# Kernel tuning notes

Hardware: AMD Instinct MI355X
Metric: run time of the kernel (lower is better)

The kernel has to match this reference:

```python
import jax, jax.numpy as jnp
import numpy as np

B, N, F_IN, F_OUT = 8, 2048, 256, 256
NEG_SLOPE = 0.2
EPS = 1e-7


def setup_inputs() -> dict:
    key = jax.random.key(0)
    k1, k2, k3, k4, k5 = jax.random.split(key, 5)
    x = jax.random.normal(k1, (B, N, F_IN), dtype=jnp.float32)
    # A is a 0/1 adjacency mask used as float in the module
    A = jax.random.bernoulli(k2, 0.5, (B, N, N)).astype(jnp.float32)
    # W: xavier_normal_ init, shape [in_features, out_features]
    W = jax.random.normal(k3, (F_IN, F_OUT), dtype=jnp.float32) * np.sqrt(2.0 / (F_IN + F_OUT))
    # attention_mechanism: Linear(2*F_OUT, 1) -> weight vector [2*F_OUT], scalar bias
    bound = 1.0 / np.sqrt(2 * F_OUT)
    a_w = jax.random.uniform(k4, (2 * F_OUT,), dtype=jnp.float32, minval=-bound, maxval=bound)
    a_b = jax.random.uniform(k5, (), dtype=jnp.float32, minval=-bound, maxval=bound)
    return {"A": A, "x": x, "W": W, "a_w": a_w, "a_b": a_b}


def reference(A, x, W, a_w, a_b):
    # Wh = x @ W : [B, N, F_OUT]
    Wh = jnp.einsum('bnf,fo->bno', x, W)
    # Linear([Wh_i ; Wh_j]) == Wh_i @ a_w[:F] + Wh_j @ a_w[F:] + b  (no O(N^2 F) concat)
    s_src = Wh @ a_w[:F_OUT]   # [B, N] contribution of row index i
    s_dst = Wh @ a_w[F_OUT:]   # [B, N] contribution of col index j
    e = s_src[:, :, None] + s_dst[:, None, :] + a_b  # [B, N, N]
    e = jnp.where(e > 0, e, NEG_SLOPE * e)           # leaky_relu(0.2)
    # masked softmax over dim=1 (as in the original module)
    exps = jnp.exp(e) * A
    sums = jnp.sum(exps, axis=1, keepdims=True) + EPS
    attn = exps / sums                                # [B, N, N]
    return jnp.einsum('bij,bjo->bio', attn, Wh)       # [B, N, F_OUT]
```

## Files before the change

kernel.cpp:

```cpp
#include <hip/hip_runtime.h>
#include <hip/hip_bf16.h>

#define NN 2048
#define BB 8
#define FD 256
#define NEG_SLOPE 0.2f
#define EPSV 1e-7f
#define PSTR 40

typedef __bf16 bf16x8 __attribute__((ext_vector_type(8)));
typedef __bf16 bf16x4 __attribute__((ext_vector_type(4)));
typedef float f32x4 __attribute__((ext_vector_type(4)));

__global__ __launch_bounds__(256) void k1_prep(const float* __restrict__ W,
                                               __bf16* __restrict__ WT) {
    int idx = blockIdx.x * 256 + threadIdx.x;
    int o = idx >> 8, f = idx & 255;
    WT[idx] = (__bf16)W[f * FD + o];
}

__global__ __launch_bounds__(256) void k2_whgemm(const float* __restrict__ x,
                                                 const __bf16* __restrict__ WT,
                                                 float* __restrict__ Wh) {
    const int wave = threadIdx.x >> 6;
    const int lane = threadIdx.x & 63;
    const int row0 = blockIdx.x * 32 + (wave >> 1) * 16;
    const int ohalf = (wave & 1) * 128;
    const int m = lane & 15;
    const int quad = lane >> 4;
    const int row = row0 + m;
    const float* xrow = x + (size_t)row * FD + quad * 8;

    f32x4 acc[8];
#pragma unroll
    for (int n = 0; n < 8; ++n) acc[n] = (f32x4){0.f, 0.f, 0.f, 0.f};

    for (int k0 = 0; k0 < FD; k0 += 32) {
        float4 xa = *(const float4*)(xrow + k0);
        float4 xb = *(const float4*)(xrow + k0 + 4);
        bf16x8 af;
        af[0] = (__bf16)xa.x; af[1] = (__bf16)xa.y; af[2] = (__bf16)xa.z; af[3] = (__bf16)xa.w;
        af[4] = (__bf16)xb.x; af[5] = (__bf16)xb.y; af[6] = (__bf16)xb.z; af[7] = (__bf16)xb.w;
#pragma unroll
        for (int n = 0; n < 8; ++n) {
            int o = ohalf + n * 16 + m;
            bf16x8 bf = *(const bf16x8*)(WT + o * FD + k0 + quad * 8);
            acc[n] = __builtin_amdgcn_mfma_f32_16x16x32_bf16(af, bf, acc[n], 0, 0, 0);
        }
    }
#pragma unroll
    for (int n = 0; n < 8; ++n) {
        int o = ohalf + n * 16 + m;
#pragma unroll
        for (int r = 0; r < 4; ++r) {
            Wh[(size_t)(row0 + quad * 4 + r) * FD + o] = acc[n][r];
        }
    }
}

__global__ __launch_bounds__(256) void k3_scores(const float* __restrict__ Wh,
                                                 const float* __restrict__ a_w,
                                                 float* __restrict__ s_src,
                                                 float* __restrict__ s_dst) {
    int wave = threadIdx.x >> 6, lane = threadIdx.x & 63;
    int row = blockIdx.x * 4 + wave;
    float4 wv = *(const float4*)(Wh + (size_t)row * FD + lane * 4);
    float4 a0 = *(const float4*)(a_w + lane * 4);
    float4 a1 = *(const float4*)(a_w + FD + lane * 4);
    float d0 = wv.x * a0.x + wv.y * a0.y + wv.z * a0.z + wv.w * a0.w;
    float d1 = wv.x * a1.x + wv.y * a1.y + wv.z * a1.z + wv.w * a1.w;
#pragma unroll
    for (int off = 32; off; off >>= 1) {
        d0 += __shfl_down(d0, off, 64);
        d1 += __shfl_down(d1, off, 64);
    }
    if (lane == 0) { s_src[row] = d0; s_dst[row] = d1; }
}

__global__ __launch_bounds__(256) void k4_den(const float* __restrict__ A,
                                              const float* __restrict__ s_src,
                                              const float* __restrict__ s_dst,
                                              const float* __restrict__ a_bp,
                                              float* __restrict__ den_part) {
    const int blk = blockIdx.x;
    const int b = blk & 7;
    const int jhalf = (blk >> 3) & 1;
    const int isp = blk >> 4;
    const int i0 = isp * 32;
    const int j = jhalf * 1024 + threadIdx.x * 4;
    __shared__ float ss[32];
    if (threadIdx.x < 32) ss[threadIdx.x] = s_src[b * NN + i0 + threadIdx.x] + a_bp[0];
    __syncthreads();
    float4 sd = *(const float4*)(s_dst + b * NN + j);
    float ax = 0.f, ay = 0.f, az = 0.f, aw = 0.f;
    const float* Ap = A + ((size_t)b * NN + i0) * NN + j;
#pragma unroll 8
    for (int i = 0; i < 32; ++i) {
        float4 a = *(const float4*)(Ap + (size_t)i * NN);
        float si = ss[i];
        float e0 = si + sd.x; e0 = e0 > 0.f ? e0 : NEG_SLOPE * e0;
        float e1 = si + sd.y; e1 = e1 > 0.f ? e1 : NEG_SLOPE * e1;
        float e2 = si + sd.z; e2 = e2 > 0.f ? e2 : NEG_SLOPE * e2;
        float e3 = si + sd.w; e3 = e3 > 0.f ? e3 : NEG_SLOPE * e3;
        ax += a.x * __expf(e0);
        ay += a.y * __expf(e1);
        az += a.z * __expf(e2);
        aw += a.w * __expf(e3);
    }
    float4 r = (float4){ax, ay, az, aw};
    *(float4*)(den_part + (size_t)isp * (BB * NN) + b * NN + j) = r;
}

__global__ __launch_bounds__(256) void k5_wht(const float* __restrict__ Wh,
                                              const float* __restrict__ den_part,
                                              __bf16* __restrict__ WhT) {
    const int b = blockIdx.z;
    const int j0 = blockIdx.x * 64;
    const int o0 = blockIdx.y * 64;
    __shared__ float tile[64][65];
    __shared__ float invd[64];
    if (threadIdx.x < 64) {
        float s = 0.f;
        const float* dp = den_part + b * NN + j0 + threadIdx.x;
#pragma unroll 8
        for (int sI = 0; sI < 64; ++sI) s += dp[(size_t)sI * (BB * NN)];
        invd[threadIdx.x] = 1.f / (s + EPSV);
    }
    __syncthreads();
    int jr = threadIdx.x >> 4, oc = (threadIdx.x & 15) * 4;
#pragma unroll
    for (int p = 0; p < 4; ++p) {
        int jj = jr + p * 16;
        float4 v = *(const float4*)(Wh + (size_t)(b * NN + j0 + jj) * FD + o0 + oc);
        float s = invd[jj];
        tile[jj][oc + 0] = v.x * s;
        tile[jj][oc + 1] = v.y * s;
        tile[jj][oc + 2] = v.z * s;
        tile[jj][oc + 3] = v.w * s;
    }
    __syncthreads();
    int ow = threadIdx.x >> 4, jc = (threadIdx.x & 15) * 4;
#pragma unroll
    for (int p = 0; p < 4; ++p) {
        int o = ow + p * 16;
        bf16x4 wv;
        wv[0] = (__bf16)tile[jc + 0][o];
        wv[1] = (__bf16)tile[jc + 1][o];
        wv[2] = (__bf16)tile[jc + 2][o];
        wv[3] = (__bf16)tile[jc + 3][o];
        *(bf16x4*)(WhT + (size_t)(b * FD + o0 + o) * NN + j0 + jc) = wv;
    }
}

__global__ __launch_bounds__(512, 4) void k6_out(const float* __restrict__ A,
                                                 const __bf16* __restrict__ WhT,
                                                 const float* __restrict__ s_src,
                                                 const float* __restrict__ s_dst,
                                                 const float* __restrict__ a_bp,
                                                 float* __restrict__ part) {
    __shared__ __bf16 P[2][128 * PSTR];
    const int blk = blockIdx.x;
    const int b = blk & 7;
    const int r_ = blk >> 3;
    const int itile = r_ & 15;
    const int jsp = r_ >> 4;
    const int i0 = itile * 128;
    const int jbase = jsp * 512;
    const int t = threadIdx.x;
    const int w = t >> 6, lane = t & 63;
    const int wrow = w >> 2, wcol = w & 3;
    const int m = lane & 15, quad = lane >> 4;

    const int prow = t >> 2, ps = t & 3;
    const float ssr = s_src[b * NN + i0 + prow] + a_bp[0];
    const float* Abase = A + ((size_t)(b * NN + i0 + prow)) * NN + jbase + ps * 8;
    const float* sdbase = s_dst + b * NN + jbase + ps * 8;
    __bf16* Pw = &P[0][0] + prow * PSTR + ps * 8;

    float4 a0 = *(const float4*)(Abase);
    float4 a1 = *(const float4*)(Abase + 4);
    float4 q0 = *(const float4*)(sdbase);
    float4 q1 = *(const float4*)(sdbase + 4);

#define BUILD_P(dstbuf)                                                          \
    {                                                                            \
        bf16x8 wv; float e;                                                      \
        e = ssr + q0.x; e = e > 0.f ? e : NEG_SLOPE * e; wv[0] = (__bf16)(a0.x * __expf(e)); \
        e = ssr + q0.y; e = e > 0.f ? e : NEG_SLOPE * e; wv[1] = (__bf16)(a0.y * __expf(e)); \
        e = ssr + q0.z; e = e > 0.f ? e : NEG_SLOPE * e; wv[2] = (__bf16)(a0.z * __expf(e)); \
        e = ssr + q0.w; e = e > 0.f ? e : NEG_SLOPE * e; wv[3] = (__bf16)(a0.w * __expf(e)); \
        e = ssr + q1.x; e = e > 0.f ? e : NEG_SLOPE * e; wv[4] = (__bf16)(a1.x * __expf(e)); \
        e = ssr + q1.y; e = e > 0.f ? e : NEG_SLOPE * e; wv[5] = (__bf16)(a1.y * __expf(e)); \
        e = ssr + q1.z; e = e > 0.f ? e : NEG_SLOPE * e; wv[6] = (__bf16)(a1.z * __expf(e)); \
        e = ssr + q1.w; e = e > 0.f ? e : NEG_SLOPE * e; wv[7] = (__bf16)(a1.w * __expf(e)); \
        *(bf16x8*)(Pw + (dstbuf) * (128 * PSTR)) = wv;                           \
    }

    BUILD_P(0)

    f32x4 acc[4][4];
#pragma unroll
    for (int r = 0; r < 4; ++r)
#pragma unroll
        for (int n = 0; n < 4; ++n) acc[r][n] = (f32x4){0.f, 0.f, 0.f, 0.f};

    const __bf16* Bbase = WhT + (size_t)(b * FD + wcol * 64 + m) * NN + jbase + quad * 8;
    const __bf16* Prd = &P[0][0] + (wrow * 64 + m) * PSTR + quad * 8;

    for (int kk = 0; kk < 16; ++kk) {
        __syncthreads();
        if (kk < 15) {
            const float* An = Abase + (kk + 1) * 32;
            const float* Sn = sdbase + (kk + 1) * 32;
            a0 = *(const float4*)(An);
            a1 = *(const float4*)(An + 4);
            q0 = *(const float4*)(Sn);
            q1 = *(const float4*)(Sn + 4);
        }
        const __bf16* Pk = Prd + (kk & 1) * (128 * PSTR);
        bf16x8 af[4];
#pragma unroll
        for (int r = 0; r < 4; ++r) af[r] = *(const bf16x8*)(Pk + r * 16 * PSTR);
#pragma unroll
        for (int n = 0; n < 4; ++n) {
            bf16x8 bfr = *(const bf16x8*)(Bbase + (size_t)(n * 16) * NN + kk * 32);
#pragma unroll
            for (int r = 0; r < 4; ++r)
                acc[r][n] = __builtin_amdgcn_mfma_f32_16x16x32_bf16(af[r], bfr, acc[r][n], 0, 0, 0);
        }
        if (kk < 15) BUILD_P((kk + 1) & 1)
    }

    float* pout = part + (size_t)jsp * (BB * NN * FD);
#pragma unroll
    for (int r = 0; r < 4; ++r) {
#pragma unroll
        for (int n = 0; n < 4; ++n) {
            int o = wcol * 64 + n * 16 + m;
#pragma unroll
            for (int rr = 0; rr < 4; ++rr) {
                int row = i0 + wrow * 64 + r * 16 + quad * 4 + rr;
                pout[(size_t)(b * NN + row) * FD + o] = acc[r][n][rr];
            }
        }
    }
#undef BUILD_P
}

__global__ __launch_bounds__(256) void k7_reduce(const float4* __restrict__ part4,
                                                 float4* __restrict__ out4) {
    int idx = blockIdx.x * 256 + threadIdx.x;
    float4 a = part4[idx];
    float4 b2 = part4[idx + 1048576];
    float4 c = part4[idx + 2097152];
    float4 d = part4[idx + 3145728];
    float4 r;
    r.x = a.x + b2.x + c.x + d.x;
    r.y = a.y + b2.y + c.y + d.y;
    r.z = a.z + b2.z + c.z + d.z;
    r.w = a.w + b2.w + c.w + d.w;
    out4[idx] = r;
}

extern "C" void kernel_launch(void* const* d_in, const int* in_sizes, int n_in,
                              void* d_out, int out_size, void* d_ws, size_t ws_size,
                              hipStream_t stream) {
    const float* A   = (const float*)d_in[0];
    const float* x   = (const float*)d_in[1];
    const float* W   = (const float*)d_in[2];
    const float* a_w = (const float*)d_in[3];
    const float* a_b = (const float*)d_in[4];
    float* out = (float*)d_out;

    char* ws = (char*)d_ws;
    __bf16* WT      = (__bf16*)ws;
    float*  Wh      = (float*)(ws + 131072);
    __bf16* WhT     = (__bf16*)(ws + 16908288);
    float*  s_src   = (float*)(ws + 25296896);
    float*  s_dst   = (float*)(ws + 25362432);
    float*  den_part= (float*)(ws + 25427968);
    float*  part    = (float*)(ws + 29622272);

    k1_prep<<<256, 256, 0, stream>>>(W, WT);
    k2_whgemm<<<512, 256, 0, stream>>>(x, WT, Wh);
    k3_scores<<<4096, 256, 0, stream>>>(Wh, a_w, s_src, s_dst);
    k4_den<<<1024, 256, 0, stream>>>(A, s_src, s_dst, a_b, den_part);
    k5_wht<<<dim3(32, 4, 8), 256, 0, stream>>>(Wh, den_part, WhT);
    k6_out<<<512, 512, 0, stream>>>(A, WhT, s_src, s_dst, a_b, part);
    k7_reduce<<<4096, 256, 0, stream>>>((const float4*)part, (float4*)out);
}
```

Baseline: 302.9 us.

## Materialize bf16 P in den kernel; stream P and WhT via global_load_lds

New measurement: 298.7 us. About the same (-1.4%).

```diff
diff --git a/kernel.cpp b/kernel.cpp
--- a/kernel.cpp
+++ b/kernel.cpp
@@ -6,11 +6,16 @@
 #define FD 256
 #define NEG_SLOPE 0.2f
 #define EPSV 1e-7f
-#define PSTR 40
 
 typedef __bf16 bf16x8 __attribute__((ext_vector_type(8)));
 typedef __bf16 bf16x4 __attribute__((ext_vector_type(4)));
 typedef float f32x4 __attribute__((ext_vector_type(4)));
+
+__device__ __forceinline__ void gload16(const __bf16* g, __bf16* l) {
+    __builtin_amdgcn_global_load_lds((const __attribute__((address_space(1))) unsigned int*)g,
+                                     (__attribute__((address_space(3))) unsigned int*)l,
+                                     16, 0, 0);
+}
 
 __global__ __launch_bounds__(256) void k1_prep(const float* __restrict__ W,
                                                __bf16* __restrict__ WT) {
@@ -81,7 +86,8 @@
                                               const float* __restrict__ s_src,
                                               const float* __restrict__ s_dst,
                                               const float* __restrict__ a_bp,
-                                              float* __restrict__ den_part) {
+                                              float* __restrict__ den_part,
+                                              __bf16* __restrict__ P) {
     const int blk = blockIdx.x;
     const int b = blk & 7;
     const int jhalf = (blk >> 3) & 1;
@@ -94,6 +100,7 @@
     float4 sd = *(const float4*)(s_dst + b * NN + j);
     float ax = 0.f, ay = 0.f, az = 0.f, aw = 0.f;
     const float* Ap = A + ((size_t)b * NN + i0) * NN + j;
+    __bf16* Pp = P + ((size_t)b * NN + i0) * NN + j;
 #pragma unroll 8
     for (int i = 0; i < 32; ++i) {
         float4 a = *(const float4*)(Ap + (size_t)i * NN);
@@ -102,10 +109,14 @@
         float e1 = si + sd.y; e1 = e1 > 0.f ? e1 : NEG_SLOPE * e1;
         float e2 = si + sd.z; e2 = e2 > 0.f ? e2 : NEG_SLOPE * e2;
         float e3 = si + sd.w; e3 = e3 > 0.f ? e3 : NEG_SLOPE * e3;
-        ax += a.x * __expf(e0);
-        ay += a.y * __expf(e1);
-        az += a.z * __expf(e2);
-        aw += a.w * __expf(e3);
+        float p0 = a.x * __expf(e0);
+        float p1 = a.y * __expf(e1);
+        float p2 = a.z * __expf(e2);
+        float p3 = a.w * __expf(e3);
+        ax += p0; ay += p1; az += p2; aw += p3;
+        bf16x4 pv;
+        pv[0] = (__bf16)p0; pv[1] = (__bf16)p1; pv[2] = (__bf16)p2; pv[3] = (__bf16)p3;
+        *(bf16x4*)(Pp + (size_t)i * NN) = pv;
     }
     float4 r = (float4){ax, ay, az, aw};
     *(float4*)(den_part + (size_t)isp * (BB * NN) + b * NN + j) = r;
@@ -152,13 +163,11 @@
     }
 }
 
-__global__ __launch_bounds__(512, 4) void k6_out(const float* __restrict__ A,
+__global__ __launch_bounds__(512, 4) void k6_out(const __bf16* __restrict__ P,
                                                  const __bf16* __restrict__ WhT,
-                                                 const float* __restrict__ s_src,
-                                                 const float* __restrict__ s_dst,
-                                                 const float* __restrict__ a_bp,
                                                  float* __restrict__ part) {
-    __shared__ __bf16 P[2][128 * PSTR];
+    __shared__ __bf16 Pt[2][128 * 32];
+    __shared__ __bf16 Bt[2][256 * 32];
     const int blk = blockIdx.x;
     const int b = blk & 7;
     const int r_ = blk >> 3;
@@ -171,32 +180,19 @@
     const int wrow = w >> 2, wcol = w & 3;
     const int m = lane & 15, quad = lane >> 4;
 
-    const int prow = t >> 2, ps = t & 3;
-    const float ssr = s_src[b * NN + i0 + prow] + a_bp[0];
-    const float* Abase = A + ((size_t)(b * NN + i0 + prow)) * NN + jbase + ps * 8;
-    const float* sdbase = s_dst + b * NN + jbase + ps * 8;
-    __bf16* Pw = &P[0][0] + prow * PSTR + ps * 8;
-
-    float4 a0 = *(const float4*)(Abase);
-    float4 a1 = *(const float4*)(Abase + 4);
-    float4 q0 = *(const float4*)(sdbase);
-    float4 q1 = *(const float4*)(sdbase + 4);
-
-#define BUILD_P(dstbuf)                                                          \
-    {                                                                            \
-        bf16x8 wv; float e;                                                      \
-        e = ssr + q0.x; e = e > 0.f ? e : NEG_SLOPE * e; wv[0] = (__bf16)(a0.x * __expf(e)); \
-        e = ssr + q0.y; e = e > 0.f ? e : NEG_SLOPE * e; wv[1] = (__bf16)(a0.y * __expf(e)); \
-        e = ssr + q0.z; e = e > 0.f ? e : NEG_SLOPE * e; wv[2] = (__bf16)(a0.z * __expf(e)); \
-        e = ssr + q0.w; e = e > 0.f ? e : NEG_SLOPE * e; wv[3] = (__bf16)(a0.w * __expf(e)); \
-        e = ssr + q1.x; e = e > 0.f ? e : NEG_SLOPE * e; wv[4] = (__bf16)(a1.x * __expf(e)); \
-        e = ssr + q1.y; e = e > 0.f ? e : NEG_SLOPE * e; wv[5] = (__bf16)(a1.y * __expf(e)); \
-        e = ssr + q1.z; e = e > 0.f ? e : NEG_SLOPE * e; wv[6] = (__bf16)(a1.z * __expf(e)); \
-        e = ssr + q1.w; e = e > 0.f ? e : NEG_SLOPE * e; wv[7] = (__bf16)(a1.w * __expf(e)); \
-        *(bf16x8*)(Pw + (dstbuf) * (128 * PSTR)) = wv;                           \
-    }
-
-    BUILD_P(0)
+    const int srow = t >> 2, schunk = t & 3;
+    const __bf16* gP  = P   + ((size_t)(b * NN + i0 + srow)) * NN + jbase + schunk * 8;
+    const __bf16* gB0 = WhT + ((size_t)(b * FD + srow)) * NN + jbase + schunk * 8;
+    const __bf16* gB1 = WhT + ((size_t)(b * FD + 128 + srow)) * NN + jbase + schunk * 8;
+    __bf16* lP  = &Pt[0][(w * 16) * 32];
+    __bf16* lB0 = &Bt[0][(w * 16) * 32];
+    __bf16* lB1 = &Bt[0][(128 + w * 16) * 32];
+    const int lstep = 128 * 32;
+    const int lstepB = 256 * 32;
+
+    gload16(gP, lP);
+    gload16(gB0, lB0);
+    gload16(gB1, lB1);
 
     f32x4 acc[4][4];
 #pragma unroll
@@ -204,31 +200,29 @@
 #pragma unroll
         for (int n = 0; n < 4; ++n) acc[r][n] = (f32x4){0.f, 0.f, 0.f, 0.f};
 
-    const __bf16* Bbase = WhT + (size_t)(b * FD + wcol * 64 + m) * NN + jbase + quad * 8;
-    const __bf16* Prd = &P[0][0] + (wrow * 64 + m) * PSTR + quad * 8;
+    const __bf16* Pr = &Pt[0][(wrow * 64 + m) * 32 + quad * 8];
+    const __bf16* Br = &Bt[0][(wcol * 64 + m) * 32 + quad * 8];
 
     for (int kk = 0; kk < 16; ++kk) {
         __syncthreads();
         if (kk < 15) {
-            const float* An = Abase + (kk + 1) * 32;
-            const float* Sn = sdbase + (kk + 1) * 32;
-            a0 = *(const float4*)(An);
-            a1 = *(const float4*)(An + 4);
-            q0 = *(const float4*)(Sn);
-            q1 = *(const float4*)(Sn + 4);
-        }
-        const __bf16* Pk = Prd + (kk & 1) * (128 * PSTR);
+            int nb = (kk + 1) & 1;
+            gload16(gP  + (kk + 1) * 32, lP  + nb * lstep);
+            gload16(gB0 + (kk + 1) * 32, lB0 + nb * lstepB);
+            gload16(gB1 + (kk + 1) * 32, lB1 + nb * lstepB);
+        }
+        const __bf16* Pk = Pr + (kk & 1) * lstep;
+        const __bf16* Bk = Br + (kk & 1) * lstepB;
         bf16x8 af[4];
 #pragma unroll
-        for (int r = 0; r < 4; ++r) af[r] = *(const bf16x8*)(Pk + r * 16 * PSTR);
+        for (int r = 0; r < 4; ++r) af[r] = *(const bf16x8*)(Pk + r * 16 * 32);
 #pragma unroll
         for (int n = 0; n < 4; ++n) {
-            bf16x8 bfr = *(const bf16x8*)(Bbase + (size_t)(n * 16) * NN + kk * 32);
+            bf16x8 bfr = *(const bf16x8*)(Bk + n * 16 * 32);
 #pragma unroll
             for (int r = 0; r < 4; ++r)
                 acc[r][n] = __builtin_amdgcn_mfma_f32_16x16x32_bf16(af[r], bfr, acc[r][n], 0, 0, 0);
         }
-        if (kk < 15) BUILD_P((kk + 1) & 1)
     }
 
     float* pout = part + (size_t)jsp * (BB * NN * FD);
@@ -244,7 +238,6 @@
             }
         }
     }
-#undef BUILD_P
 }
 
 __global__ __launch_bounds__(256) void k7_reduce(const float4* __restrict__ part4,
@@ -279,13 +272,14 @@
     float*  s_src   = (float*)(ws + 25296896);
     float*  s_dst   = (float*)(ws + 25362432);
     float*  den_part= (float*)(ws + 25427968);
-    float*  part    = (float*)(ws + 29622272);
+    __bf16* P       = (__bf16*)(ws + 29622272);
+    float*  part    = (float*)(ws + 96731136);
 
     k1_prep<<<256, 256, 0, stream>>>(W, WT);
     k2_whgemm<<<512, 256, 0, stream>>>(x, WT, Wh);
     k3_scores<<<4096, 256, 0, stream>>>(Wh, a_w, s_src, s_dst);
-    k4_den<<<1024, 256, 0, stream>>>(A, s_src, s_dst, a_b, den_part);
+    k4_den<<<1024, 256, 0, stream>>>(A, s_src, s_dst, a_b, den_part, P);
     k5_wht<<<dim3(32, 4, 8), 256, 0, stream>>>(Wh, den_part, WhT);
-    k6_out<<<512, 512, 0, stream>>>(A, WhT, s_src, s_dst, a_b, part);
+    k6_out<<<512, 512, 0, stream>>>(P, WhT, part);
     k7_reduce<<<4096, 256, 0, stream>>>((const float4*)part, (float4*)out);
 }
```

## Drop split-K partials and stage WhT tiles into LDS via direct global-to-LDS loads

Applied to the files above, without the earlier changes.

New measurement: 306.4 us. No clear change (+1.1%).

```diff
diff --git a/kernel.cpp b/kernel.cpp
--- a/kernel.cpp
+++ b/kernel.cpp
@@ -6,11 +6,17 @@
 #define FD 256
 #define NEG_SLOPE 0.2f
 #define EPSV 1e-7f
-#define PSTR 40
+#define PSTR 36
 
 typedef __bf16 bf16x8 __attribute__((ext_vector_type(8)));
 typedef __bf16 bf16x4 __attribute__((ext_vector_type(4)));
 typedef float f32x4 __attribute__((ext_vector_type(4)));
+
+__device__ __forceinline__ void gload16(const __bf16* g, __bf16* l) {
+    __builtin_amdgcn_global_load_lds((const __attribute__((address_space(1))) unsigned int*)g,
+                                     (__attribute__((address_space(3))) unsigned int*)l,
+                                     16, 0, 0);
+}
 
 __global__ __launch_bounds__(256) void k1_prep(const float* __restrict__ W,
                                                __bf16* __restrict__ WT) {
@@ -152,114 +158,98 @@
     }
 }
 
-__global__ __launch_bounds__(512, 4) void k6_out(const float* __restrict__ A,
-                                                 const __bf16* __restrict__ WhT,
-                                                 const float* __restrict__ s_src,
-                                                 const float* __restrict__ s_dst,
-                                                 const float* __restrict__ a_bp,
-                                                 float* __restrict__ part) {
-    __shared__ __bf16 P[2][128 * PSTR];
+__global__ __launch_bounds__(256) void k6_out(const float* __restrict__ A,
+                                              const __bf16* __restrict__ WhT,
+                                              const float* __restrict__ s_src,
+                                              const float* __restrict__ s_dst,
+                                              const float* __restrict__ a_bp,
+                                              float* __restrict__ out) {
+    __shared__ __bf16 Pt[2][32 * PSTR];
+    __shared__ __bf16 Bt[2][256 * 32];
     const int blk = blockIdx.x;
     const int b = blk & 7;
-    const int r_ = blk >> 3;
-    const int itile = r_ & 15;
-    const int jsp = r_ >> 4;
-    const int i0 = itile * 128;
-    const int jbase = jsp * 512;
+    const int itile = blk >> 3;
+    const int i0 = itile * 32;
     const int t = threadIdx.x;
     const int w = t >> 6, lane = t & 63;
-    const int wrow = w >> 2, wcol = w & 3;
     const int m = lane & 15, quad = lane >> 4;
 
-    const int prow = t >> 2, ps = t & 3;
+    const int prow = t >> 3, pj = (t & 7) * 4;
     const float ssr = s_src[b * NN + i0 + prow] + a_bp[0];
-    const float* Abase = A + ((size_t)(b * NN + i0 + prow)) * NN + jbase + ps * 8;
-    const float* sdbase = s_dst + b * NN + jbase + ps * 8;
-    __bf16* Pw = &P[0][0] + prow * PSTR + ps * 8;
+    const float* Abase = A + ((size_t)(b * NN + i0 + prow)) * NN + pj;
+    const float* sdbase = s_dst + b * NN + pj;
+    __bf16* Pw = &Pt[0][0] + prow * PSTR + pj;
+    const int pstep = 32 * PSTR;
+
+    const int srow = t >> 2, schunk = t & 3;
+    const __bf16* gB = WhT + ((size_t)(b * FD + srow)) * NN + schunk * 8;
+    __bf16* lB = &Bt[0][(w * 16) * 32];
+    const int lstepB = 256 * 32;
 
     float4 a0 = *(const float4*)(Abase);
-    float4 a1 = *(const float4*)(Abase + 4);
     float4 q0 = *(const float4*)(sdbase);
-    float4 q1 = *(const float4*)(sdbase + 4);
+#pragma unroll
+    for (int c = 0; c < 4; ++c) gload16(gB + (size_t)(c * 64) * NN, lB + c * 64 * 32);
 
 #define BUILD_P(dstbuf)                                                          \
     {                                                                            \
-        bf16x8 wv; float e;                                                      \
-        e = ssr + q0.x; e = e > 0.f ? e : NEG_SLOPE * e; wv[0] = (__bf16)(a0.x * __expf(e)); \
-        e = ssr + q0.y; e = e > 0.f ? e : NEG_SLOPE * e; wv[1] = (__bf16)(a0.y * __expf(e)); \
-        e = ssr + q0.z; e = e > 0.f ? e : NEG_SLOPE * e; wv[2] = (__bf16)(a0.z * __expf(e)); \
-        e = ssr + q0.w; e = e > 0.f ? e : NEG_SLOPE * e; wv[3] = (__bf16)(a0.w * __expf(e)); \
-        e = ssr + q1.x; e = e > 0.f ? e : NEG_SLOPE * e; wv[4] = (__bf16)(a1.x * __expf(e)); \
-        e = ssr + q1.y; e = e > 0.f ? e : NEG_SLOPE * e; wv[5] = (__bf16)(a1.y * __expf(e)); \
-        e = ssr + q1.z; e = e > 0.f ? e : NEG_SLOPE * e; wv[6] = (__bf16)(a1.z * __expf(e)); \
-        e = ssr + q1.w; e = e > 0.f ? e : NEG_SLOPE * e; wv[7] = (__bf16)(a1.w * __expf(e)); \
-        *(bf16x8*)(Pw + (dstbuf) * (128 * PSTR)) = wv;                           \
+        bf16x4 pv; float e;                                                      \
+        e = ssr + q0.x; e = e > 0.f ? e : NEG_SLOPE * e; pv[0] = (__bf16)(a0.x * __expf(e)); \
+        e = ssr + q0.y; e = e > 0.f ? e : NEG_SLOPE * e; pv[1] = (__bf16)(a0.y * __expf(e)); \
+        e = ssr + q0.z; e = e > 0.f ? e : NEG_SLOPE * e; pv[2] = (__bf16)(a0.z * __expf(e)); \
+        e = ssr + q0.w; e = e > 0.f ? e : NEG_SLOPE * e; pv[3] = (__bf16)(a0.w * __expf(e)); \
+        *(bf16x4*)(Pw + (dstbuf) * pstep) = pv;                                  \
     }
 
     BUILD_P(0)
 
-    f32x4 acc[4][4];
-#pragma unroll
-    for (int r = 0; r < 4; ++r)
+    f32x4 acc[2][4];
+#pragma unroll
+    for (int r = 0; r < 2; ++r)
 #pragma unroll
         for (int n = 0; n < 4; ++n) acc[r][n] = (f32x4){0.f, 0.f, 0.f, 0.f};
 
-    const __bf16* Bbase = WhT + (size_t)(b * FD + wcol * 64 + m) * NN + jbase + quad * 8;
-    const __bf16* Prd = &P[0][0] + (wrow * 64 + m) * PSTR + quad * 8;
-
-    for (int kk = 0; kk < 16; ++kk) {
+    const __bf16* Pr = &Pt[0][m * PSTR + quad * 8];
+    const __bf16* Br = &Bt[0][(w * 64 + m) * 32 + quad * 8];
+
+    for (int kk = 0; kk < 64; ++kk) {
         __syncthreads();
-        if (kk < 15) {
-            const float* An = Abase + (kk + 1) * 32;
-            const float* Sn = sdbase + (kk + 1) * 32;
-            a0 = *(const float4*)(An);
-            a1 = *(const float4*)(An + 4);
-            q0 = *(const float4*)(Sn);
-            q1 = *(const float4*)(Sn + 4);
-        }
-        const __bf16* Pk = Prd + (kk & 1) * (128 * PSTR);
-        bf16x8 af[4];
-#pragma unroll
-        for (int r = 0; r < 4; ++r) af[r] = *(const bf16x8*)(Pk + r * 16 * PSTR);
+        const int cur = kk & 1, nb = cur ^ 1;
+        if (kk < 63) {
+#pragma unroll
+            for (int c = 0; c < 4; ++c)
+                gload16(gB + (size_t)(c * 64) * NN + (kk + 1) * 32, lB + nb * lstepB + c * 64 * 32);
+            a0 = *(const float4*)(Abase + (kk + 1) * 32);
+            q0 = *(const float4*)(sdbase + (kk + 1) * 32);
+        }
+        const __bf16* Pk = Pr + cur * pstep;
+        const __bf16* Bk = Br + cur * lstepB;
+        bf16x8 af[2];
+        af[0] = *(const bf16x8*)(Pk);
+        af[1] = *(const bf16x8*)(Pk + 16 * PSTR);
 #pragma unroll
         for (int n = 0; n < 4; ++n) {
-            bf16x8 bfr = *(const bf16x8*)(Bbase + (size_t)(n * 16) * NN + kk * 32);
-#pragma unroll
-            for (int r = 0; r < 4; ++r)
+            bf16x8 bfr = *(const bf16x8*)(Bk + n * 16 * 32);
+#pragma unroll
+            for (int r = 0; r < 2; ++r)
                 acc[r][n] = __builtin_amdgcn_mfma_f32_16x16x32_bf16(af[r], bfr, acc[r][n], 0, 0, 0);
         }
-        if (kk < 15) BUILD_P((kk + 1) & 1)
-    }
-
-    float* pout = part + (size_t)jsp * (BB * NN * FD);
-#pragma unroll
-    for (int r = 0; r < 4; ++r) {
+        if (kk < 63) BUILD_P(nb)
+    }
+
+#pragma unroll
+    for (int r = 0; r < 2; ++r) {
 #pragma unroll
         for (int n = 0; n < 4; ++n) {
-            int o = wcol * 64 + n * 16 + m;
+            int o = w * 64 + n * 16 + m;
 #pragma unroll
             for (int rr = 0; rr < 4; ++rr) {
-                int row = i0 + wrow * 64 + r * 16 + quad * 4 + rr;
-                pout[(size_t)(b * NN + row) * FD + o] = acc[r][n][rr];
+                int row = i0 + r * 16 + quad * 4 + rr;
+                out[((size_t)b * NN + row) * FD + o] = acc[r][n][rr];
             }
         }
     }
 #undef BUILD_P
-}
-
-__global__ __launch_bounds__(256) void k7_reduce(const float4* __restrict__ part4,
-                                                 float4* __restrict__ out4) {
-    int idx = blockIdx.x * 256 + threadIdx.x;
-    float4 a = part4[idx];
-    float4 b2 = part4[idx + 1048576];
-    float4 c = part4[idx + 2097152];
-    float4 d = part4[idx + 3145728];
-    float4 r;
-    r.x = a.x + b2.x + c.x + d.x;
-    r.y = a.y + b2.y + c.y + d.y;
-    r.z = a.z + b2.z + c.z + d.z;
-    r.w = a.w + b2.w + c.w + d.w;
-    out4[idx] = r;
 }
 
 extern "C" void kernel_launch(void* const* d_in, const int* in_sizes, int n_in,
@@ -279,13 +269,11 @@
     float*  s_src   = (float*)(ws + 25296896);
     float*  s_dst   = (float*)(ws + 25362432);
     float*  den_part= (float*)(ws + 25427968);
-    float*  part    = (float*)(ws + 29622272);
 
     k1_prep<<<256, 256, 0, stream>>>(W, WT);
     k2_whgemm<<<512, 256, 0, stream>>>(x, WT, Wh);
     k3_scores<<<4096, 256, 0, stream>>>(Wh, a_w, s_src, s_dst);
     k4_den<<<1024, 256, 0, stream>>>(A, s_src, s_dst, a_b, den_part);
     k5_wht<<<dim3(32, 4, 8), 256, 0, stream>>>(Wh, den_part, WhT);
-    k6_out<<<512, 512, 0, stream>>>(A, WhT, s_src, s_dst, a_b, part);
-    k7_reduce<<<4096, 256, 0, stream>>>((const float4*)part, (float4*)out);
-}
+    k6_out<<<512, 256, 0, stream>>>(A, WhT, s_src, s_dst, a_b, out);
+}
```
